# Performance work log

Measured on AMD Instinct MI355X. Metric: run time of the kernel, lower is better.

## Reference

```python
import jax, jax.numpy as jnp
import numpy as np

N_NODES = 4096
F_UAV = 64
N_OBS = N_NODES * F_UAV + 256  # 262400
H = 1024
N_ACT = 64
N_EDGES = 65536


def setup_inputs() -> dict:
    key = jax.random.key(0)
    ks = jax.random.split(key, 13)
    s = lambda fan_in: 1.0 / np.sqrt(fan_in)
    return {
        "node_x": jax.random.normal(ks[0], (N_NODES, F_UAV), jnp.float32),
        "flat_obs": jax.random.normal(ks[1], (N_OBS,), jnp.float32),
        "gcn_w": jax.random.normal(ks[2], (F_UAV, F_UAV), jnp.float32) * s(F_UAV),
        "gcn_b": jnp.zeros((F_UAV,), jnp.float32),
        "w1": jax.random.normal(ks[3], (N_OBS, H), jnp.float32) * s(N_OBS),
        "b1": jnp.zeros((H,), jnp.float32),
        "w2": jax.random.normal(ks[4], (H, H), jnp.float32) * s(H),
        "b2": jnp.zeros((H,), jnp.float32),
        "wv": jax.random.normal(ks[5], (H, 1), jnp.float32) * s(H),
        "bv": jnp.zeros((1,), jnp.float32),
        "wa": jax.random.normal(ks[6], (H, N_ACT), jnp.float32) * s(H),
        "ba": jnp.zeros((N_ACT,), jnp.float32),
        "edge_index": jax.random.randint(ks[7], (2, N_EDGES), 0, N_NODES, jnp.int64),
    }


def _gcn_conv(x, edge_index, w, b):
    n = x.shape[0]
    loops = jnp.arange(n, dtype=edge_index.dtype)
    src = jnp.concatenate([edge_index[0], loops])
    dst = jnp.concatenate([edge_index[1], loops])
    deg = jax.ops.segment_sum(jnp.ones_like(dst, dtype=x.dtype), dst, num_segments=n)
    dinv = jax.lax.rsqrt(deg)  # deg >= 1 thanks to self-loops
    norm = dinv[src] * dinv[dst]          # [E+N]
    h = x @ w                              # [N, F]
    msg = h[src] * norm[:, None]           # gather + scale
    out = jax.ops.segment_sum(msg, dst, num_segments=n)  # scatter-add
    return out + b


def reference(node_x, flat_obs, gcn_w, gcn_b, w1, b1, w2, b2, wv, bv, wa, ba, edge_index):
    y_uav = _gcn_conv(node_x, edge_index, gcn_w, gcn_b).reshape(-1)  # flatten
    x = jnp.concatenate([y_uav, flat_obs[y_uav.shape[0]:]], axis=0)  # [N_OBS]
    y = jax.nn.relu(x @ w1 + b1)
    y = jax.nn.relu(y @ w2 + b2)
    value = y @ wv + bv                    # [1]
    adv = y @ wa + ba                      # [N_ACT]
    return value + adv - jnp.mean(adv, keepdims=True)
```

## Files before the change

### kernel.cpp

```cpp
#include <hip/hip_runtime.h>

#define N_NODES 4096
#define F_UAV 64
#define NOBS 262400
#define GCN_FLAT (N_NODES * F_UAV)
#define HDIM 1024
#define N_ACT 64
#define N_EDGES 65536
#define NBUCKET 64

typedef float f32x4 __attribute__((ext_vector_type(4)));
typedef float f32x2 __attribute__((ext_vector_type(2)));

#define OFF_CUR    0
#define OFF_SSRC   (OFF_CUR + N_NODES)
#define OFF_H      (OFF_SSRC + N_NODES * NBUCKET)
#define OFF_P1     (OFF_H + GCN_FLAT)
#define OFF_Q1T    (OFF_P1 + 2048 * HDIM)
#define OFF_P2     (OFF_Q1T + HDIM * 128)

__global__ __launch_bounds__(256) void k_gcn_h(const float* __restrict__ nx,
                                               const float* __restrict__ w,
                                               const int* __restrict__ src,
                                               const int* __restrict__ dst,
                                               float* __restrict__ h,
                                               int* __restrict__ cur,
                                               int* __restrict__ ssrc) {
    __shared__ float sw[F_UAV * F_UAV];
    __shared__ float sx4[256];
    int tid = threadIdx.x;
    for (int i = tid; i < F_UAV * F_UAV; i += 256) sw[i] = w[i];
    sx4[tid] = nx[blockIdx.x * 256 + tid];
    if (blockIdx.x < 256) {
        int e = blockIdx.x * 256 + tid;
        int d = dst[e];
        int slot = atomicAdd(&cur[d], 1);
        if (slot < NBUCKET) ssrc[d * NBUCKET + slot] = src[e];
    }
    __syncthreads();
    int r = tid >> 6, j = tid & 63;
    float acc = 0.f;
#pragma unroll
    for (int k = 0; k < F_UAV; ++k) acc += sx4[r * 64 + k] * sw[k * F_UAV + j];
    h[blockIdx.x * 256 + r * 64 + j] = acc;
}

__global__ __launch_bounds__(256) void k_mv1g(const float* __restrict__ h,
                                              const int* __restrict__ cur,
                                              const int* __restrict__ ssrc,
                                              const float* __restrict__ gb,
                                              const float* __restrict__ obs,
                                              const float* __restrict__ W,
                                              float* __restrict__ part) {
    __shared__ float sxa[128];
    __shared__ float sx[129];
    int tid = threadIdx.x, b = blockIdx.x;
    int w = tid >> 6, l = tid & 63;
    if (tid < 128) sxa[tid] = 0.f;
    __syncthreads();
    {
        int n = 2 * b + (w >> 1);
        int deg = cur[n];
        int dm = deg < NBUCKET ? deg : NBUCKET;
        float a0 = 0.f;
        for (int i = (w & 1); i < dm; i += 2) {
            int s = ssrc[n * NBUCKET + i];
            a0 += h[s * 64 + l] * rsqrtf((float)(cur[s] + 1));
        }
        atomicAdd(&sxa[(w >> 1) * 64 + l], a0);
    }
    __syncthreads();
    if (tid < 128) {
        int nn = 2 * b + (tid >> 6);
        float di = rsqrtf((float)(cur[nn] + 1));
        sx[tid] = di * sxa[tid] + di * di * h[nn * 64 + (tid & 63)] + gb[tid & 63];
    }
    if (tid == 128) sx[128] = (b < 256) ? obs[GCN_FLAT + b] : 0.f;
    __syncthreads();
    f32x4 acc = {0.f, 0.f, 0.f, 0.f};
    const f32x4* Wr = (const f32x4*)W + (size_t)(b * 128) * (HDIM / 4) + tid;
    for (int k = 0; k < 128; k += 8) {
#pragma unroll
        for (int u = 0; u < 8; ++u)
            acc += sx[k + u] * __builtin_nontemporal_load(&Wr[(size_t)(k + u) * (HDIM / 4)]);
    }
    if (b < 256) {
        const f32x4* wt = (const f32x4*)W + (size_t)(GCN_FLAT + b) * (HDIM / 4) + tid;
        acc += sx[128] * __builtin_nontemporal_load(wt);
    }
    ((f32x4*)(part + (size_t)b * HDIM))[tid] = acc;
}

template <int NSEG>
__global__ __launch_bounds__(256) void k_sum16T(const float* __restrict__ part,
                                                float* __restrict__ qT) {
    int t = threadIdx.x, s = blockIdx.x;
    const f32x4* p = ((const f32x4*)part) + (size_t)s * 16 * (HDIM / 4) + t;
    f32x4 acc = {0.f, 0.f, 0.f, 0.f};
#pragma unroll
    for (int r = 0; r < 16; ++r) acc += p[(size_t)r * (HDIM / 4)];
#pragma unroll
    for (int u = 0; u < 4; ++u) qT[(size_t)(4 * t + u) * NSEG + s] = acc[u];
}

__global__ __launch_bounds__(256) void k_fin_mv2(const float* __restrict__ q1T,
                                                 const float* __restrict__ b1,
                                                 const float* __restrict__ w2,
                                                 float* __restrict__ p2) {
    __shared__ float s_y[16];
    int t = threadIdx.x, b = blockIdx.x;
    int w = t >> 6, l = t & 63;
#pragma unroll
    for (int rr = 0; rr < 4; ++rr) {
        int j = 16 * b + 4 * w + rr;
        f32x2 v = *(const f32x2*)&q1T[(size_t)j * 128 + 2 * l];
        float sm = v.x + v.y;
        for (int off = 32; off; off >>= 1) sm += __shfl_xor(sm, off);
        if (l == 0) s_y[4 * w + rr] = fmaxf(b1[j] + sm, 0.f);
    }
    __syncthreads();
    f32x4 acc = {0.f, 0.f, 0.f, 0.f};
    const f32x4* Wr = ((const f32x4*)w2) + (size_t)(16 * b) * (HDIM / 4) + t;
#pragma unroll
    for (int i = 0; i < 16; ++i) acc += s_y[i] * Wr[(size_t)i * (HDIM / 4)];
    ((f32x4*)(p2 + (size_t)b * HDIM))[t] = acc;
}

__global__ __launch_bounds__(1024) void k_heads_f(const float* __restrict__ p2,
                                                  const float* __restrict__ b2,
                                                  const float* __restrict__ wv,
                                                  const float* __restrict__ bv,
                                                  const float* __restrict__ wa,
                                                  const float* __restrict__ ba,
                                                  float* __restrict__ out) {
    __shared__ float y2s[1024];
    __shared__ float s_adv[16][64];
    __shared__ float s_pv[1024];
    int t = threadIdx.x;
    float acc = b2[t];
#pragma unroll 8
    for (int s = 0; s < 64; ++s) acc += p2[s * HDIM + t];
    float y = fmaxf(acc, 0.f);
    y2s[t] = y;
    s_pv[t] = y * wv[t];
    __syncthreads();
    int g = t >> 6, a = t & 63;
    float pa = 0.f;
#pragma unroll 4
    for (int kk = 0; kk < 64; ++kk) pa += y2s[g * 64 + kk] * wa[(g * 64 + kk) * 64 + a];
    s_adv[g][a] = pa;
    __syncthreads();
    if (t < 64) {
        float adv = ba[a];
#pragma unroll
        for (int gg = 0; gg < 16; ++gg) adv += s_adv[gg][a];
        float v = 0.f;
#pragma unroll
        for (int i = 0; i < 16; ++i) v += s_pv[a + 64 * i];
        for (int off = 32; off; off >>= 1) v += __shfl_xor(v, off);
        float m = adv;
        for (int off = 32; off; off >>= 1) m += __shfl_xor(m, off);
        m *= (1.f / 64.f);
        out[a] = (v + bv[0]) + adv - m;
    }
}

extern "C" void kernel_launch(void* const* d_in, const int* in_sizes, int n_in,
                              void* d_out, int out_size, void* d_ws, size_t ws_size,
                              hipStream_t stream) {
    const float* node_x   = (const float*)d_in[0];
    const float* flat_obs = (const float*)d_in[1];
    const float* gcn_w    = (const float*)d_in[2];
    const float* gcn_b    = (const float*)d_in[3];
    const float* w1       = (const float*)d_in[4];
    const float* b1       = (const float*)d_in[5];
    const float* w2       = (const float*)d_in[6];
    const float* b2       = (const float*)d_in[7];
    const float* wv       = (const float*)d_in[8];
    const float* bv       = (const float*)d_in[9];
    const float* wa       = (const float*)d_in[10];
    const float* ba       = (const float*)d_in[11];
    const int*   ei       = (const int*)d_in[12];
    const int* src = ei;
    const int* dst = ei + N_EDGES;

    int* wsi = (int*)d_ws;
    float* wsf = (float*)d_ws;
    int*   cur  = wsi + OFF_CUR;
    int*   ssrc = wsi + OFF_SSRC;
    float* h    = wsf + OFF_H;
    float* p1   = wsf + OFF_P1;
    float* q1T  = wsf + OFF_Q1T;
    float* p2   = wsf + OFF_P2;
    float* out  = (float*)d_out;

    hipMemsetAsync(cur, 0, N_NODES * sizeof(int), stream);
    k_gcn_h<<<GCN_FLAT / 256, 256, 0, stream>>>(node_x, gcn_w, src, dst, h, cur, ssrc);
    k_mv1g<<<2048, 256, 0, stream>>>(h, cur, ssrc, gcn_b, flat_obs, w1, p1);
    k_sum16T<128><<<128, 256, 0, stream>>>(p1, q1T);
    k_fin_mv2<<<64, 256, 0, stream>>>(q1T, b1, w2, p2);
    k_heads_f<<<1, 1024, 0, stream>>>(p2, b2, wv, bv, wa, ba, out);
}
```

Baseline: 210.5 us.

## Reorder GCN to aggregate raw features then apply weight inside mv1 kernel

Uses (A_norm X) W = A_norm (X W) to skip the separate X@W pass. The first kernel now only places edges into per-node buckets. The main matvec kernel gathers raw node features, normalizes them, then multiplies its two nodes by the 64x64 GCN weight held in shared memory. This removes the write and re-read of the h buffer and shrinks the first kernel, at the cost of a 16KB weight load into shared memory and a small matmul in each of the 2048 blocks.

```diff
diff --git a/kernel.cpp b/kernel.cpp
--- a/kernel.cpp
+++ b/kernel.cpp
@@ -14,49 +14,35 @@
 
 #define OFF_CUR    0
 #define OFF_SSRC   (OFF_CUR + N_NODES)
-#define OFF_H      (OFF_SSRC + N_NODES * NBUCKET)
-#define OFF_P1     (OFF_H + GCN_FLAT)
+#define OFF_P1     (OFF_SSRC + N_NODES * NBUCKET)
 #define OFF_Q1T    (OFF_P1 + 2048 * HDIM)
 #define OFF_P2     (OFF_Q1T + HDIM * 128)
 
-__global__ __launch_bounds__(256) void k_gcn_h(const float* __restrict__ nx,
-                                               const float* __restrict__ w,
-                                               const int* __restrict__ src,
+__global__ __launch_bounds__(256) void k_place(const int* __restrict__ src,
                                                const int* __restrict__ dst,
-                                               float* __restrict__ h,
                                                int* __restrict__ cur,
                                                int* __restrict__ ssrc) {
-    __shared__ float sw[F_UAV * F_UAV];
-    __shared__ float sx4[256];
-    int tid = threadIdx.x;
-    for (int i = tid; i < F_UAV * F_UAV; i += 256) sw[i] = w[i];
-    sx4[tid] = nx[blockIdx.x * 256 + tid];
-    if (blockIdx.x < 256) {
-        int e = blockIdx.x * 256 + tid;
-        int d = dst[e];
-        int slot = atomicAdd(&cur[d], 1);
-        if (slot < NBUCKET) ssrc[d * NBUCKET + slot] = src[e];
-    }
-    __syncthreads();
-    int r = tid >> 6, j = tid & 63;
-    float acc = 0.f;
-#pragma unroll
-    for (int k = 0; k < F_UAV; ++k) acc += sx4[r * 64 + k] * sw[k * F_UAV + j];
-    h[blockIdx.x * 256 + r * 64 + j] = acc;
+    int e = blockIdx.x * 256 + threadIdx.x;
+    int d = dst[e];
+    int slot = atomicAdd(&cur[d], 1);
+    if (slot < NBUCKET) ssrc[d * NBUCKET + slot] = src[e];
 }
 
-__global__ __launch_bounds__(256) void k_mv1g(const float* __restrict__ h,
+__global__ __launch_bounds__(256) void k_mv1g(const float* __restrict__ nx,
                                               const int* __restrict__ cur,
                                               const int* __restrict__ ssrc,
+                                              const float* __restrict__ gw,
                                               const float* __restrict__ gb,
                                               const float* __restrict__ obs,
                                               const float* __restrict__ W,
                                               float* __restrict__ part) {
-    __shared__ float sxa[128];
+    __shared__ float sgw[F_UAV * F_UAV];
+    __shared__ float sv[128];
     __shared__ float sx[129];
     int tid = threadIdx.x, b = blockIdx.x;
     int w = tid >> 6, l = tid & 63;
-    if (tid < 128) sxa[tid] = 0.f;
+    for (int i = tid; i < F_UAV * F_UAV; i += 256) sgw[i] = gw[i];
+    if (tid < 128) sv[tid] = 0.f;
     __syncthreads();
     {
         int n = 2 * b + (w >> 1);
@@ -65,15 +51,23 @@
         float a0 = 0.f;
         for (int i = (w & 1); i < dm; i += 2) {
             int s = ssrc[n * NBUCKET + i];
-            a0 += h[s * 64 + l] * rsqrtf((float)(cur[s] + 1));
+            a0 += nx[s * 64 + l] * rsqrtf((float)(cur[s] + 1));
         }
-        atomicAdd(&sxa[(w >> 1) * 64 + l], a0);
+        atomicAdd(&sv[(w >> 1) * 64 + l], a0);
     }
     __syncthreads();
     if (tid < 128) {
-        int nn = 2 * b + (tid >> 6);
-        float di = rsqrtf((float)(cur[nn] + 1));
-        sx[tid] = di * sxa[tid] + di * di * h[nn * 64 + (tid & 63)] + gb[tid & 63];
+        int n = 2 * b + (tid >> 6);
+        float di = rsqrtf((float)(cur[n] + 1));
+        sv[tid] = di * sv[tid] + di * di * nx[n * 64 + (tid & 63)];
+    }
+    __syncthreads();
+    if (tid < 128) {
+        int q = tid >> 6, j = tid & 63;
+        float xv = gb[j];
+#pragma unroll 8
+        for (int k = 0; k < 64; ++k) xv += sv[q * 64 + k] * sgw[k * 64 + j];
+        sx[tid] = xv;
     }
     if (tid == 128) sx[128] = (b < 256) ? obs[GCN_FLAT + b] : 0.f;
     __syncthreads();
@@ -188,15 +182,15 @@
     float* wsf = (float*)d_ws;
     int*   cur  = wsi + OFF_CUR;
     int*   ssrc = wsi + OFF_SSRC;
-    float* h    = wsf + OFF_H;
     float* p1   = wsf + OFF_P1;
     float* q1T  = wsf + OFF_Q1T;
     float* p2   = wsf + OFF_P2;
     float* out  = (float*)d_out;
 
     hipMemsetAsync(cur, 0, N_NODES * sizeof(int), stream);
-    k_gcn_h<<<GCN_FLAT / 256, 256, 0, stream>>>(node_x, gcn_w, src, dst, h, cur, ssrc);
-    k_mv1g<<<2048, 256, 0, stream>>>(h, cur, ssrc, gcn_b, flat_obs, w1, p1);
+    k_place<<<N_EDGES / 256, 256, 0, stream>>>(src, dst, cur, ssrc);
+    k_mv1g<<<2048, 256, 0, stream>>>(node_x, cur, ssrc, gcn_w, gcn_b,
+                                     flat_obs, w1, p1);
     k_sum16T<128><<<128, 256, 0, stream>>>(p1, q1T);
     k_fin_mv2<<<64, 256, 0, stream>>>(q1T, b1, w2, p2);
     k_heads_f<<<1, 1024, 0, stream>>>(p2, b2, wv, bv, wa, ba, out);
```

New measurement: 209.5 us. No clear change (-0.5%).
